# Optimization experiments

Hardware: AMD Instinct MI355X
Metric: run time of the kernel (lower is better)

The kernel has to match this reference:

```python
import jax, jax.numpy as jnp
import numpy as np

DIM = 256; K = 3; PAD = 1; DIL = 1; B = 16; H = 56; W = 56
SP = 8           # share_planes
RADIX = 2
ATTN = max(DIM * RADIX // 4, 32)   # 128
EMB = K * K * DIM // SP            # 288

def conv(x, w, pad=0, dil=1, groups=1):
    return jax.lax.conv_general_dilated(
        x, w, (1, 1), [(pad, pad), (pad, pad)], rhs_dilation=(dil, dil),
        feature_group_count=groups, dimension_numbers=('NCHW', 'OIHW', 'NCHW'))

def bn(x, g, b, m, v, eps=1e-5):
    # eval-mode BatchNorm2d
    s = g * jax.lax.rsqrt(v + eps)
    return x * s[None, :, None, None] + (b - m * s)[None, :, None, None]

def gn(x, g, b, groups, eps=1e-5):
    Bb, C, Hh, Ww = x.shape
    xg = x.reshape(Bb, groups, C // groups, Hh, Ww)
    mu = xg.mean((2, 3, 4), keepdims=True)
    var = xg.var((2, 3, 4), keepdims=True)
    xg = (xg - mu) * jax.lax.rsqrt(var + eps)
    return xg.reshape(Bb, C, Hh, Ww) * g[None, :, None, None] + b[None, :, None, None]

def unfold3(x):
    # im2col for 3x3, stride 1, pad 1 -> (B, C, K*K, H, W)
    Bb, C, Hh, Ww = x.shape
    p = (K - 1) // 2
    xp = jnp.pad(x, ((0, 0), (0, 0), (p, p), (p, p)))
    return jnp.stack([xp[:, :, i:i + Hh, j:j + Ww] for i in range(K) for j in range(K)], axis=2)

def reference(x, ke_w, ke_g, ke_b, ke_m, ke_v, e1_w, e1_g, e1_b, e1_m, e1_v,
              e2_w, e2_b, gng, gnb, c1_w, c1_g, c1_b, c1_m, c1_v,
              b2_g, b2_b, b2_m, b2_v, s1_w, s1_b, s1_g, s1_bb, s1_m, s1_v,
              s2_w, s2_b):
    Bb = x.shape[0]
    # key embed: grouped kxk conv + BN + ReLU
    k = jax.nn.relu(bn(conv(x, ke_w, pad=PAD, dil=DIL, groups=4), ke_g, ke_b, ke_m, ke_v))
    qk = jnp.concatenate([x, k], axis=1)                     # (B, 2*DIM, H, W)
    # dynamic kernel branch
    wemb = jax.nn.relu(bn(conv(qk, e1_w), e1_g, e1_b, e1_m, e1_v))
    wemb = conv(wemb, e2_w) + e2_b[None, :, None, None]
    wemb = gn(wemb, gng, gnb, DIM // SP)                     # GroupNorm(dim//8 groups)
    wemb = wemb.reshape(Bb, DIM // SP, K * K, H, W)
    # value branch
    xq = bn(conv(x, c1_w), c1_g, c1_b, c1_m, c1_v)
    # local dynamic convolution: per-pixel kernel shared across SP channels
    patches = unfold3(xq).reshape(Bb, DIM // SP, SP, K * K, H, W)
    y = (patches * wemb[:, :, None]).sum(3).reshape(Bb, DIM, H, W)
    y = bn(y, b2_g, b2_b, b2_m, b2_v)
    y = y * jax.nn.sigmoid(y)                                # swish
    # split attention over radix=2 branches (y, k)
    xs = jnp.stack([y, k], axis=2)                           # (B, C, 2, H, W)
    gap = xs.sum(2).mean((2, 3), keepdims=True)              # (B, C, 1, 1)
    a = jax.nn.relu(bn(conv(gap, s1_w) + s1_b[None, :, None, None], s1_g, s1_bb, s1_m, s1_v))
    a = conv(a, s2_w) + s2_b[None, :, None, None]            # (B, 2*C, 1, 1)
    a = jax.nn.softmax(a.reshape(Bb, DIM, RADIX), axis=2)
    out = (xs * a[:, :, :, None, None]).sum(2)
    return out

def setup_inputs():
    key = jax.random.key(0)
    ks = iter(jax.random.split(key, 40))
    def n(shape, s=1.0):
        return jax.random.normal(next(ks), shape, jnp.float32) * s
    def u(shape):
        return jax.random.uniform(next(ks), shape, jnp.float32, minval=0.5, maxval=1.5)
    d = {}
    d['x'] = n((B, DIM, H, W))
    d['ke_w'] = n((DIM, DIM // 4, K, K), 0.05)
    d['ke_g'] = u((DIM,)); d['ke_b'] = n((DIM,), 0.1); d['ke_m'] = n((DIM,), 0.1); d['ke_v'] = u((DIM,))
    d['e1_w'] = n((DIM // 2, 2 * DIM, 1, 1), 0.05)
    d['e1_g'] = u((DIM // 2,)); d['e1_b'] = n((DIM // 2,), 0.1); d['e1_m'] = n((DIM // 2,), 0.1); d['e1_v'] = u((DIM // 2,))
    d['e2_w'] = n((EMB, DIM // 2, 1, 1), 0.05); d['e2_b'] = n((EMB,), 0.1)
    d['gng'] = u((EMB,)); d['gnb'] = n((EMB,), 0.1)
    d['c1_w'] = n((DIM, DIM, 1, 1), 0.05)
    d['c1_g'] = u((DIM,)); d['c1_b'] = n((DIM,), 0.1); d['c1_m'] = n((DIM,), 0.1); d['c1_v'] = u((DIM,))
    d['b2_g'] = u((DIM,)); d['b2_b'] = n((DIM,), 0.1); d['b2_m'] = n((DIM,), 0.1); d['b2_v'] = u((DIM,))
    d['s1_w'] = n((ATTN, DIM, 1, 1), 0.05); d['s1_b'] = n((ATTN,), 0.1)
    d['s1_g'] = u((ATTN,)); d['s1_bb'] = n((ATTN,), 0.1); d['s1_m'] = n((ATTN,), 0.1); d['s1_v'] = u((ATTN,))
    d['s2_w'] = n((RADIX * DIM, ATTN, 1, 1), 0.05); d['s2_b'] = n((RADIX * DIM,), 0.1)
    return d
```

## Files before the change

### kernel.cpp

```cpp
#include <hip/hip_runtime.h>
#include <hip/hip_bf16.h>

typedef __hip_bfloat16 bf16;
typedef float f32x4 __attribute__((ext_vector_type(4)));
typedef short s16x8 __attribute__((ext_vector_type(8)));

#define NPIX 3136
#define HDIM 56
#define CDIM 256

static __device__ __forceinline__ float b2f(bf16 v){ return __bfloat162float(v); }
static __device__ __forceinline__ bf16  f2b(float v){ return __float2bfloat16(v); }

#define O_KE_S 0
#define O_KE_B 256
#define O_E1_S 512
#define O_E1_B 640
#define O_C1_S 768
#define O_C1_B 1024
#define O_B2_S 1280
#define O_B2_B 1536
#define O_S1_S 1792
#define O_S1_B 1920
#define O_E2B  2048
#define O_GNS  2336
#define O_GAP  3360
#define O_ATT  7456

__global__ void prep(
    const float* __restrict__ kew, const float* __restrict__ e1w,
    const float* __restrict__ e2w, const float* __restrict__ c1w,
    const float* keg, const float* keb, const float* kem, const float* kev,
    const float* e1g, const float* e1b, const float* e1m, const float* e1v,
    const float* e2b,
    const float* c1g, const float* c1b, const float* c1m, const float* c1v,
    const float* b2g, const float* b2b, const float* b2m, const float* b2v,
    const float* s1g, const float* s1bb, const float* s1m, const float* s1v,
    bf16* kewT, bf16* e1wb, bf16* e2wb, bf16* c1wb, float* o)
{
    int bid = blockIdx.x, t = threadIdx.x;
    if (bid < 576) {
        int i = bid * 256 + t;
        int ci = i & 63, co_l = (i >> 6) & 63;
        int gt = i >> 12;
        int tap = gt % 9, g = gt / 9;
        int co = g * 64 + co_l;
        kewT[i] = f2b(kew[(co * 64 + ci) * 9 + tap]);
    } else if (bid < 832) {
        int i = (bid - 576) * 256 + t; e1wb[i] = f2b(e1w[i]);
    } else if (bid < 976) {
        int i = (bid - 832) * 256 + t; e2wb[i] = f2b(e2w[i]);
    } else if (bid < 1232) {
        int i = (bid - 976) * 256 + t; c1wb[i] = f2b(c1w[i]);
    } else if (bid == 1232) {
        const float eps = 1e-5f;
        {
            float s = keg[t] * rsqrtf(kev[t] + eps);
            o[O_KE_S + t] = s; o[O_KE_B + t] = keb[t] - kem[t] * s;
            s = c1g[t] * rsqrtf(c1v[t] + eps);
            o[O_C1_S + t] = s; o[O_C1_B + t] = c1b[t] - c1m[t] * s;
            s = b2g[t] * rsqrtf(b2v[t] + eps);
            o[O_B2_S + t] = s; o[O_B2_B + t] = b2b[t] - b2m[t] * s;
        }
        if (t < 128) {
            float s = e1g[t] * rsqrtf(e1v[t] + eps);
            o[O_E1_S + t] = s; o[O_E1_B + t] = e1b[t] - e1m[t] * s;
            s = s1g[t] * rsqrtf(s1v[t] + eps);
            o[O_S1_S + t] = s; o[O_S1_B + t] = s1bb[t] - s1m[t] * s;
        }
        for (int i = t; i < 288; i += 256) o[O_E2B + i] = e2b[i];
    } else {
        int j = (bid - 1233) * 256 + t;
        if (j < 1024) o[O_GNS + j] = 0.f;
        else          o[O_GAP + j - 1024] = 0.f;
    }
}

__global__ __launch_bounds__(256) void cvt_x(const float* __restrict__ x, bf16* __restrict__ xh)
{
    int b = blockIdx.y;
    int p0 = blockIdx.x * 64;
    __shared__ bf16 T[64][264];
    int t = threadIdx.x;
    for (int it = 0; it < 16; it++) {
        int slot = t + it * 256;
        int c = slot >> 4, ch4 = slot & 15;
        float4 v = *(const float4*)(x + ((long)b * CDIM + c) * NPIX + p0 + ch4 * 4);
        T[ch4 * 4 + 0][c] = f2b(v.x);
        T[ch4 * 4 + 1][c] = f2b(v.y);
        T[ch4 * 4 + 2][c] = f2b(v.z);
        T[ch4 * 4 + 3][c] = f2b(v.w);
    }
    __syncthreads();
    for (int it = 0; it < 8; it++) {
        int slot = t + it * 256;
        int p = slot >> 5, cc = slot & 31;
        *(float4*)(xh + ((long)b * NPIX + p0 + p) * CDIM + cc * 8) = *(const float4*)&T[p][cc * 8];
    }
}

__global__ __launch_bounds__(256) void gconv_mfma(
    const bf16* __restrict__ xh, const bf16* __restrict__ wT,
    const float* __restrict__ scale, const float* __restrict__ bias,
    bf16* __restrict__ kh)
{
    int b = blockIdx.z, g = blockIdx.y;
    int p0 = blockIdx.x * 64;
    __shared__ bf16 As[5 * 58 * 72];
    int t = threadIdx.x;
    int wv = t >> 6, lane = t & 63, q = lane >> 4, ln = lane & 15;
    int r_first = p0 / HDIM - 1;

    #pragma unroll
    for (int i = 0; i < 10; i++) {
        int slot = t + i * 256;
        if (slot < 2320) {
            int chunk = slot & 7, pos = slot >> 3;
            int ri = pos / 58, ci = pos - ri * 58;
            int h = r_first + ri, w = ci - 1;
            float4 v = {0.f, 0.f, 0.f, 0.f};
            if ((unsigned)h < HDIM && (unsigned)w < HDIM)
                v = *(const float4*)(xh + ((long)b * NPIX + h * HDIM + w) * CDIM + g * 64 + chunk * 8);
            *(float4*)&As[pos * 72 + chunk * 8] = v;
        }
    }
    __syncthreads();

    int posp[4];
    #pragma unroll
    for (int pt = 0; pt < 4; pt++) {
        int p = p0 + pt * 16 + ln;
        int hp = p / HDIM, wp = p - hp * HDIM;
        posp[pt] = (hp - r_first) * 58 + wp + 1;
    }
    const bf16* wbase = wT + ((long)(g * 9) * 64 + wv * 16 + ln) * 64;

    f32x4 acc[4] = {};
    #pragma unroll
    for (int tap = 0; tap < 9; tap++) {
        int dpos = (tap / 3 - 1) * 58 + (tap % 3 - 1);
        const bf16* wp = wbase + tap * 64 * 64;
        s16x8 B0 = *(const s16x8*)(wp + q * 8);
        s16x8 B1 = *(const s16x8*)(wp + 32 + q * 8);
        #pragma unroll
        for (int pt = 0; pt < 4; pt++) {
            int base = (posp[pt] + dpos) * 72 + q * 8;
            s16x8 a0 = *(const s16x8*)&As[base];
            s16x8 a1 = *(const s16x8*)&As[base + 32];
            acc[pt] = __builtin_amdgcn_mfma_f32_16x16x32_bf16(a0, B0, acc[pt], 0, 0, 0);
            acc[pt] = __builtin_amdgcn_mfma_f32_16x16x32_bf16(a1, B1, acc[pt], 0, 0, 0);
        }
    }

    __syncthreads();
    int co = g * 64 + wv * 16 + ln;
    float sc = scale[co], bi = bias[co];
    #pragma unroll
    for (int pt = 0; pt < 4; pt++)
        #pragma unroll
        for (int r = 0; r < 4; r++)
            As[(pt * 16 + q * 4 + r) * 72 + wv * 16 + ln] = f2b(fmaxf(acc[pt][r] * sc + bi, 0.f));
    __syncthreads();
    #pragma unroll
    for (int i = 0; i < 2; i++) {
        int slot = t + i * 256;
        int row = slot >> 3, cc = slot & 7;
        *(float4*)(kh + ((long)b * NPIX + p0 + row) * CDIM + g * 64 + cc * 8) = *(const float4*)&As[row * 72 + cc * 8];
    }
}

template<int MODE>
__global__ __launch_bounds__(256) void mfma_gemm(
    const bf16* __restrict__ Wt, const bf16* __restrict__ X0, const bf16* __restrict__ X1,
    int C0, int K, int M,
    const float* __restrict__ scale, const float* __restrict__ bias,
    bf16* __restrict__ Y, float* __restrict__ gnsum)
{
    int b = blockIdx.z;
    int p0 = blockIdx.x * 64;
    int m0 = blockIdx.y * 128;
    __shared__ bf16 SH[64 * 72 + 128 * 72];
    bf16* As = SH;
    bf16* Bs = SH + 64 * 72;
    __shared__ float gs[64];
    int t = threadIdx.x;
    int wv = t >> 6, lane = t & 63, q = lane >> 4, ln = lane & 15;
    if (MODE == 1) { if (t < 64) gs[t] = 0.f; }

    f32x4 acc[4][2] = {};
    for (int k0 = 0; k0 < K; k0 += 64) {
        __syncthreads();
        #pragma unroll
        for (int i = 0; i < 2; i++) {
            int slot = t + i * 256;
            int chunk = slot & 7, row = slot >> 3;
            int ch = k0 + chunk * 8;
            const bf16* src = (ch < C0)
                ? X0 + ((long)b * NPIX + p0 + row) * C0 + ch
                : X1 + ((long)b * NPIX + p0 + row) * (K - C0) + (ch - C0);
            *(float4*)&As[row * 72 + chunk * 8] = *(const float4*)src;
        }
        #pragma unroll
        for (int i = 0; i < 4; i++) {
            int slot = t + i * 256;
            int chunk = slot & 7, row = slot >> 3;
            int m = m0 + row;
            float4 v = {0.f, 0.f, 0.f, 0.f};
            if (m < M) v = *(const float4*)(Wt + (long)m * K + k0 + chunk * 8);
            *(float4*)&Bs[row * 72 + chunk * 8] = v;
        }
        __syncthreads();
        #pragma unroll
        for (int kk = 0; kk < 2; kk++) {
            s16x8 a[4];
            #pragma unroll
            for (int pt = 0; pt < 4; pt++)
                a[pt] = *(const s16x8*)&As[(pt * 16 + ln) * 72 + kk * 32 + q * 8];
            #pragma unroll
            for (int mi = 0; mi < 2; mi++) {
                s16x8 bb = *(const s16x8*)&Bs[(wv * 32 + mi * 16 + ln) * 72 + kk * 32 + q * 8];
                #pragma unroll
                for (int pt = 0; pt < 4; pt++)
                    acc[pt][mi] = __builtin_amdgcn_mfma_f32_16x16x32_bf16(a[pt], bb, acc[pt][mi], 0, 0, 0);
            }
        }
    }

    __syncthreads();
    bf16* T = SH;
    #pragma unroll
    for (int mi = 0; mi < 2; mi++) {
        int m = m0 + wv * 32 + mi * 16 + ln;
        int mc = (m > M - 1) ? (M - 1) : m;
        float sc = 1.f, bi;
        if (MODE == 0 || MODE == 2) { sc = scale[mc]; bi = bias[mc]; }
        else bi = bias[mc];
        float ps = 0.f, pq = 0.f;
        #pragma unroll
        for (int pt = 0; pt < 4; pt++) {
            #pragma unroll
            for (int r = 0; r < 4; r++) {
                float v = acc[pt][mi][r] * sc + bi;
                if (MODE == 0) v = fmaxf(v, 0.f);
                if (MODE == 1) { ps += v; pq += v * v; }
                T[(pt * 16 + q * 4 + r) * 144 + wv * 32 + mi * 16 + ln] = f2b(v);
            }
        }
        if (MODE == 1 && m < M) {
            int grp = m / 9;
            atomicAdd(&gs[grp * 2], ps);
            atomicAdd(&gs[grp * 2 + 1], pq);
        }
    }
    __syncthreads();
    #pragma unroll
    for (int i = 0; i < 4; i++) {
        int slot = t + i * 256;
        int chunk = slot & 15, row = slot >> 4;
        int m = m0 + chunk * 8;
        if (m + 8 <= M)
            *(float4*)(Y + ((long)b * NPIX + p0 + row) * M + m) = *(const float4*)&T[row * 144 + chunk * 8];
    }
    if (MODE == 1 && t < 64) atomicAdd(&gnsum[b * 64 + t], gs[t]);
}

__global__ __launch_bounds__(256) void dynconv(
    const bf16* __restrict__ xq, const bf16* __restrict__ wemb,
    const float* __restrict__ gnsum,
    const float* __restrict__ gng, const float* __restrict__ gnb,
    const float* __restrict__ b2s, const float* __restrict__ b2b,
    bf16* __restrict__ y)
{
    int id = blockIdx.x * 256 + threadIdx.x;
    int grp = id & 31;
    int p = (id >> 5) % NPIX;
    int b = id / (NPIX * 32);
    int h = p / HDIM, w = p % HDIM;
    float S = gnsum[b * 64 + grp * 2], Q = gnsum[b * 64 + grp * 2 + 1];
    float mu = S * (1.f / 28224.f);
    float var = Q * (1.f / 28224.f) - mu * mu;
    float rs = rsqrtf(fmaxf(var, 0.f) + 1e-5f);
    const bf16* wp = wemb + ((long)b * NPIX + p) * 288 + grp * 9;
    float wv[9];
    #pragma unroll
    for (int tp = 0; tp < 9; tp++)
        wv[tp] = (b2f(wp[tp]) - mu) * rs * gng[grp * 9 + tp] + gnb[grp * 9 + tp];
    float acc[8] = {};
    #pragma unroll
    for (int tp = 0; tp < 9; tp++) {
        int h2 = h + tp / 3 - 1, w2 = w + tp % 3 - 1;
        if ((unsigned)h2 >= HDIM || (unsigned)w2 >= HDIM) continue;
        const bf16* xp = xq + ((long)b * NPIX + h2 * HDIM + w2) * CDIM + grp * 8;
        s16x8 xv = *(const s16x8*)xp;
        const bf16* xb = (const bf16*)&xv;
        float wt = wv[tp];
        #pragma unroll
        for (int i = 0; i < 8; i++) acc[i] += b2f(xb[i]) * wt;
    }
    bf16 outv[8];
    #pragma unroll
    for (int i = 0; i < 8; i++) {
        int c = grp * 8 + i;
        float v = acc[i] * b2s[c] + b2b[c];
        outv[i] = f2b(v / (1.f + __expf(-v)));
    }
    *(float4*)(y + ((long)b * NPIX + p) * CDIM + grp * 8) = *(const float4*)outv;
}

__global__ void gapk(const bf16* __restrict__ y, const bf16* __restrict__ k, float* __restrict__ gap)
{
    int b = blockIdx.x, chunk = blockIdx.y, c = threadIdx.x;
    float s = 0.f;
    for (int i = 0; i < 64; i++) {
        long off = ((long)b * NPIX + chunk * 64 + i) * CDIM + c;
        s += b2f(y[off]) + b2f(k[off]);
    }
    atomicAdd(&gap[b * 256 + c], s * (1.f / NPIX));
}

__global__ void attnk(const float* __restrict__ gap,
                      const float* __restrict__ s1w, const float* __restrict__ s1b,
                      const float* __restrict__ s1s, const float* __restrict__ s1bi,
                      const float* __restrict__ s2w, const float* __restrict__ s2b,
                      float* __restrict__ att)
{
    int b = blockIdx.x, t = threadIdx.x;
    __shared__ float g[256], a1[128];
    for (int i = t; i < 256; i += 128) g[i] = gap[b * 256 + i];
    __syncthreads();
    float s = 0.f;
    for (int ci = 0; ci < 256; ci++) s += s1w[t * 256 + ci] * g[ci];
    s += s1b[t];
    s = s * s1s[t] + s1bi[t];
    a1[t] = fmaxf(s, 0.f);
    __syncthreads();
    for (int c = t; c < 256; c += 128) {
        float v0 = s2b[2 * c], v1 = s2b[2 * c + 1];
        for (int ci = 0; ci < 128; ci++) {
            float av = a1[ci];
            v0 += s2w[(2 * c) * 128 + ci] * av;
            v1 += s2w[(2 * c + 1) * 128 + ci] * av;
        }
        float m = fmaxf(v0, v1);
        float e0 = __expf(v0 - m), e1 = __expf(v1 - m);
        float inv = 1.f / (e0 + e1);
        att[(b * 256 + c) * 2 + 0] = e0 * inv;
        att[(b * 256 + c) * 2 + 1] = e1 * inv;
    }
}

__global__ __launch_bounds__(256) void finalk(
    const bf16* __restrict__ y, const bf16* __restrict__ k,
    const float* __restrict__ att, float* __restrict__ out)
{
    int b = blockIdx.z, c0 = blockIdx.y * 64, p0 = blockIdx.x * 64;
    __shared__ bf16 Ys[64][72], Ks[64][72];
    int t = threadIdx.x;
    #pragma unroll
    for (int i = 0; i < 2; i++) {
        int slot = t + i * 256;
        int row = slot >> 3, cc = slot & 7;
        long off = ((long)b * NPIX + p0 + row) * CDIM + c0 + cc * 8;
        *(float4*)&Ys[row][cc * 8] = *(const float4*)(y + off);
        *(float4*)&Ks[row][cc * 8] = *(const float4*)(k + off);
    }
    __syncthreads();
    int c_l = t >> 2, pc = t & 3;
    int c = c0 + c_l;
    float a0 = att[(b * 256 + c) * 2], a1 = att[(b * 256 + c) * 2 + 1];
    float4 o[4];
    float* of = (float*)o;
    #pragma unroll
    for (int j = 0; j < 16; j++) {
        int p = pc * 16 + j;
        of[j] = b2f(Ys[p][c_l]) * a0 + b2f(Ks[p][c_l]) * a1;
    }
    float* dst = out + ((long)b * CDIM + c) * NPIX + p0 + pc * 16;
    #pragma unroll
    for (int j = 0; j < 4; j++) ((float4*)dst)[j] = o[j];
}

extern "C" void kernel_launch(void* const* d_in, const int* in_sizes, int n_in,
                              void* d_out, int out_size, void* d_ws, size_t ws_size,
                              hipStream_t stream)
{
    const float* x    = (const float*)d_in[0];
    const float* ke_w = (const float*)d_in[1];
    const float* ke_g = (const float*)d_in[2];
    const float* ke_b = (const float*)d_in[3];
    const float* ke_m = (const float*)d_in[4];
    const float* ke_v = (const float*)d_in[5];
    const float* e1_w = (const float*)d_in[6];
    const float* e1_g = (const float*)d_in[7];
    const float* e1_b = (const float*)d_in[8];
    const float* e1_m = (const float*)d_in[9];
    const float* e1_v = (const float*)d_in[10];
    const float* e2_w = (const float*)d_in[11];
    const float* e2_b = (const float*)d_in[12];
    const float* gng  = (const float*)d_in[13];
    const float* gnb  = (const float*)d_in[14];
    const float* c1_w = (const float*)d_in[15];
    const float* c1_g = (const float*)d_in[16];
    const float* c1_b = (const float*)d_in[17];
    const float* c1_m = (const float*)d_in[18];
    const float* c1_v = (const float*)d_in[19];
    const float* b2_g = (const float*)d_in[20];
    const float* b2_b = (const float*)d_in[21];
    const float* b2_m = (const float*)d_in[22];
    const float* b2_v = (const float*)d_in[23];
    const float* s1_w = (const float*)d_in[24];
    const float* s1_b = (const float*)d_in[25];
    const float* s1_g = (const float*)d_in[26];
    const float* s1_bb= (const float*)d_in[27];
    const float* s1_m = (const float*)d_in[28];
    const float* s1_v = (const float*)d_in[29];
    const float* s2_w = (const float*)d_in[30];
    const float* s2_b = (const float*)d_in[31];

    float* fold = (float*)d_ws;
    bf16* wsb   = (bf16*)((char*)d_ws + 65536);
    bf16* xh   = wsb;
    bf16* kh   = xh + 12845056L;
    bf16* wemb = kh + 12845056L;
    bf16* w1   = wemb + 14450688L;
    bf16* xq   = w1;
    bf16* yb   = xh;
    bf16* kewT = w1 + 12845056L;
    bf16* e1wb = kewT + 147456L;
    bf16* e2wb = e1wb + 65536L;
    bf16* c1wb = e2wb + 36864L;

    prep<<<dim3(1253), dim3(256), 0, stream>>>(
        ke_w, e1_w, e2_w, c1_w,
        ke_g, ke_b, ke_m, ke_v, e1_g, e1_b, e1_m, e1_v, e2_b,
        c1_g, c1_b, c1_m, c1_v, b2_g, b2_b, b2_m, b2_v,
        s1_g, s1_bb, s1_m, s1_v,
        kewT, e1wb, e2wb, c1wb, fold);

    cvt_x<<<dim3(49, 16), dim3(256), 0, stream>>>(x, xh);

    gconv_mfma<<<dim3(49, 4, 16), dim3(256), 0, stream>>>(
        xh, kewT, fold + O_KE_S, fold + O_KE_B, kh);

    mfma_gemm<0><<<dim3(49, 1, 16), dim3(256), 0, stream>>>(
        e1wb, xh, kh, 256, 512, 128, fold + O_E1_S, fold + O_E1_B, w1, nullptr);

    mfma_gemm<1><<<dim3(49, 3, 16), dim3(256), 0, stream>>>(
        e2wb, w1, (const bf16*)nullptr, 128, 128, 288, (const float*)nullptr, fold + O_E2B,
        wemb, fold + O_GNS);

    mfma_gemm<2><<<dim3(49, 2, 16), dim3(256), 0, stream>>>(
        c1wb, xh, (const bf16*)nullptr, 256, 256, 256, fold + O_C1_S, fold + O_C1_B, xq, nullptr);

    dynconv<<<dim3(6272), dim3(256), 0, stream>>>(
        xq, wemb, fold + O_GNS, gng, gnb,
        fold + O_B2_S, fold + O_B2_B, yb);

    gapk<<<dim3(16, 49), dim3(256), 0, stream>>>(yb, kh, fold + O_GAP);

    attnk<<<dim3(16), dim3(128), 0, stream>>>(
        fold + O_GAP, s1_w, s1_b, fold + O_S1_S, fold + O_S1_B, s2_w, s2_b, fold + O_ATT);

    finalk<<<dim3(49, 4, 16), dim3(256), 0, stream>>>(yb, kh, fold + O_ATT, (float*)d_out);
}
```

Measured before the change: 366.6 us.

## Fuse global average pooling into grouped conv and dynconv epilogues

```diff
diff --git a/kernel.cpp b/kernel.cpp
--- a/kernel.cpp
+++ b/kernel.cpp
@@ -102,22 +102,22 @@
 __global__ __launch_bounds__(256) void gconv_mfma(
     const bf16* __restrict__ xh, const bf16* __restrict__ wT,
     const float* __restrict__ scale, const float* __restrict__ bias,
-    bf16* __restrict__ kh)
+    bf16* __restrict__ kh, float* __restrict__ gap)
 {
     int b = blockIdx.z, g = blockIdx.y;
-    int p0 = blockIdx.x * 64;
-    __shared__ bf16 As[5 * 58 * 72];
+    int tr = blockIdx.x / 7, tc = blockIdx.x % 7;
+    int h0 = tr * 8, w0 = tc * 8;
+    __shared__ bf16 As[100 * 72];
     int t = threadIdx.x;
     int wv = t >> 6, lane = t & 63, q = lane >> 4, ln = lane & 15;
-    int r_first = p0 / HDIM - 1;
-
-    #pragma unroll
-    for (int i = 0; i < 10; i++) {
+
+    #pragma unroll
+    for (int i = 0; i < 4; i++) {
         int slot = t + i * 256;
-        if (slot < 2320) {
+        if (slot < 800) {
             int chunk = slot & 7, pos = slot >> 3;
-            int ri = pos / 58, ci = pos - ri * 58;
-            int h = r_first + ri, w = ci - 1;
+            int ri = pos / 10, ci = pos - ri * 10;
+            int h = h0 - 1 + ri, w = w0 - 1 + ci;
             float4 v = {0.f, 0.f, 0.f, 0.f};
             if ((unsigned)h < HDIM && (unsigned)w < HDIM)
                 v = *(const float4*)(xh + ((long)b * NPIX + h * HDIM + w) * CDIM + g * 64 + chunk * 8);
@@ -129,16 +129,15 @@
     int posp[4];
     #pragma unroll
     for (int pt = 0; pt < 4; pt++) {
-        int p = p0 + pt * 16 + ln;
-        int hp = p / HDIM, wp = p - hp * HDIM;
-        posp[pt] = (hp - r_first) * 58 + wp + 1;
+        int o = pt * 16 + ln;
+        posp[pt] = ((o >> 3) + 1) * 10 + (o & 7) + 1;
     }
     const bf16* wbase = wT + ((long)(g * 9) * 64 + wv * 16 + ln) * 64;
 
     f32x4 acc[4] = {};
     #pragma unroll
     for (int tap = 0; tap < 9; tap++) {
-        int dpos = (tap / 3 - 1) * 58 + (tap % 3 - 1);
+        int dpos = (tap / 3 - 1) * 10 + (tap % 3 - 1);
         const bf16* wp = wbase + tap * 64 * 64;
         s16x8 B0 = *(const s16x8*)(wp + q * 8);
         s16x8 B1 = *(const s16x8*)(wp + 32 + q * 8);
@@ -155,17 +154,25 @@
     __syncthreads();
     int co = g * 64 + wv * 16 + ln;
     float sc = scale[co], bi = bias[co];
+    float ksum = 0.f;
     #pragma unroll
     for (int pt = 0; pt < 4; pt++)
         #pragma unroll
-        for (int r = 0; r < 4; r++)
-            As[(pt * 16 + q * 4 + r) * 72 + wv * 16 + ln] = f2b(fmaxf(acc[pt][r] * sc + bi, 0.f));
+        for (int r = 0; r < 4; r++) {
+            float v = fmaxf(acc[pt][r] * sc + bi, 0.f);
+            ksum += v;
+            As[(pt * 16 + q * 4 + r) * 72 + wv * 16 + ln] = f2b(v);
+        }
+    ksum += __shfl_xor(ksum, 16);
+    ksum += __shfl_xor(ksum, 32);
+    if (lane < 16) atomicAdd(&gap[b * 256 + co], ksum * (1.f / NPIX));
     __syncthreads();
     #pragma unroll
     for (int i = 0; i < 2; i++) {
         int slot = t + i * 256;
         int row = slot >> 3, cc = slot & 7;
-        *(float4*)(kh + ((long)b * NPIX + p0 + row) * CDIM + g * 64 + cc * 8) = *(const float4*)&As[row * 72 + cc * 8];
+        int h = h0 + (row >> 3), w = w0 + (row & 7);
+        *(float4*)(kh + ((long)b * NPIX + h * HDIM + w) * CDIM + g * 64 + cc * 8) = *(const float4*)&As[row * 72 + cc * 8];
     }
 }
 
@@ -269,7 +276,7 @@
     const float* __restrict__ gnsum,
     const float* __restrict__ gng, const float* __restrict__ gnb,
     const float* __restrict__ b2s, const float* __restrict__ b2b,
-    bf16* __restrict__ y)
+    bf16* __restrict__ y, float* __restrict__ gap)
 {
     int id = blockIdx.x * 256 + threadIdx.x;
     int grp = id & 31;
@@ -298,24 +305,28 @@
         for (int i = 0; i < 8; i++) acc[i] += b2f(xb[i]) * wt;
     }
     bf16 outv[8];
+    float lv[8];
     #pragma unroll
     for (int i = 0; i < 8; i++) {
         int c = grp * 8 + i;
         float v = acc[i] * b2s[c] + b2b[c];
-        outv[i] = f2b(v / (1.f + __expf(-v)));
+        v = v / (1.f + __expf(-v));
+        lv[i] = v;
+        outv[i] = f2b(v);
     }
     *(float4*)(y + ((long)b * NPIX + p) * CDIM + grp * 8) = *(const float4*)outv;
-}
-
-__global__ void gapk(const bf16* __restrict__ y, const bf16* __restrict__ k, float* __restrict__ gap)
-{
-    int b = blockIdx.x, chunk = blockIdx.y, c = threadIdx.x;
-    float s = 0.f;
-    for (int i = 0; i < 64; i++) {
-        long off = ((long)b * NPIX + chunk * 64 + i) * CDIM + c;
-        s += b2f(y[off]) + b2f(k[off]);
-    }
-    atomicAdd(&gap[b * 256 + c], s * (1.f / NPIX));
+
+    __shared__ float gsh[4 * 256];
+    int t = threadIdx.x, wvi = t >> 6, l = t & 63;
+    #pragma unroll
+    for (int i = 0; i < 8; i++) lv[i] += __shfl_xor(lv[i], 32);
+    if (l < 32) {
+        #pragma unroll
+        for (int i = 0; i < 8; i++) gsh[wvi * 256 + l * 8 + i] = lv[i];
+    }
+    __syncthreads();
+    float s = gsh[t] + gsh[256 + t] + gsh[512 + t] + gsh[768 + t];
+    atomicAdd(&gap[b * 256 + t], s * (1.f / NPIX));
 }
 
 __global__ void attnk(const float* __restrict__ gap,
@@ -440,7 +451,7 @@
     cvt_x<<<dim3(49, 16), dim3(256), 0, stream>>>(x, xh);
 
     gconv_mfma<<<dim3(49, 4, 16), dim3(256), 0, stream>>>(
-        xh, kewT, fold + O_KE_S, fold + O_KE_B, kh);
+        xh, kewT, fold + O_KE_S, fold + O_KE_B, kh, fold + O_GAP);
 
     mfma_gemm<0><<<dim3(49, 1, 16), dim3(256), 0, stream>>>(
         e1wb, xh, kh, 256, 512, 128, fold + O_E1_S, fold + O_E1_B, w1, nullptr);
@@ -454,9 +465,7 @@
 
     dynconv<<<dim3(6272), dim3(256), 0, stream>>>(
         xq, wemb, fold + O_GNS, gng, gnb,
-        fold + O_B2_S, fold + O_B2_B, yb);
-
-    gapk<<<dim3(16, 49), dim3(256), 0, stream>>>(yb, kh, fold + O_GAP);
+        fold + O_B2_S, fold + O_B2_B, yb, fold + O_GAP);
 
     attnk<<<dim3(16), dim3(128), 0, stream>>>(
         fold + O_GAP, s1_w, s1_b, fold + O_S1_S, fold + O_S1_B, s2_w, s2_b, fold + O_ATT);
```

After: 368.2 us. About the same (+0.4%).
